# Kernel tuning notes

Measured on AMD Instinct MI355X. Metric: run time of the kernel, lower is better.

The kernel has to match this reference:

```python
import jax, jax.numpy as jnp
import numpy as np

D_MODEL = 512
N_HEADS = 8
D_HEAD = D_MODEL // N_HEADS
EPS = 1e-5


def layer_norm(x, g, b):
    mu = jnp.mean(x, axis=-1, keepdims=True)
    var = jnp.mean(jnp.square(x - mu), axis=-1, keepdims=True)
    return (x - mu) * jax.lax.rsqrt(var + EPS) * g + b


def setup_inputs() -> dict:
    key = jax.random.key(0)
    ks = jax.random.split(key, 8)
    B, L, D = 2, 4096, D_MODEL
    x = jax.random.normal(ks[0], (B, L, D), dtype=jnp.float32)
    # monotonically increasing event timestamps (hours)
    timestamps = jnp.sort(jax.random.uniform(ks[1], (B, L), dtype=jnp.float32) * 1000.0, axis=-1)
    mask = jnp.ones((B, L), dtype=jnp.float32)
    s = 0.02
    return {
        "x": x,
        "timestamps": timestamps,
        "mask": mask,
        "ln1_g": jnp.ones((D,), jnp.float32),
        "ln1_b": jnp.zeros((D,), jnp.float32),
        "w_qkv": jax.random.normal(ks[2], (3 * D, D), jnp.float32) * s,
        "w_out": jax.random.normal(ks[3], (D, D), jnp.float32) * s,
        "decay_rate": jnp.ones((N_HEADS,), jnp.float32) * 0.01,
        "ln2_g": jnp.ones((D,), jnp.float32),
        "ln2_b": jnp.zeros((D,), jnp.float32),
        "w_ff1": jax.random.normal(ks[4], (4 * D, D), jnp.float32) * s,
        "w_ff2": jax.random.normal(ks[5], (D, 4 * D), jnp.float32) * s,
    }


def reference(x, timestamps, mask, ln1_g, ln1_b, w_qkv, w_out, decay_rate, ln2_g, ln2_b, w_ff1, w_ff2):
    B, L, D = x.shape
    H, dh = N_HEADS, D_HEAD
    scale = dh ** (-0.5)

    xn = layer_norm(x, ln1_g, ln1_b)
    qkv = (xn @ w_qkv.T).reshape(B, L, 3, H, dh).transpose(2, 0, 3, 1, 4)  # [3,B,H,L,dh]
    q, k, v = qkv[0], qkv[1], qkv[2]

    attn = jnp.einsum("bhid,bhjd->bhij", q, k) * scale  # [B,H,L,L]

    # temporal-decay bias
    t_diff = jnp.abs(timestamps[:, None, :, None] - timestamps[:, None, None, :]) / 24.0  # [B,1,L,L]
    decay = jax.nn.softplus(decay_rate)[None, :, None, None]  # [1,H,1,1]
    attn = attn - decay * t_diff

    # causal mask
    causal = jnp.triu(jnp.ones((L, L), dtype=bool), k=1)
    attn = jnp.where(causal[None, None], -jnp.inf, attn)

    # padding mask over keys
    pad = (mask == 0)[:, None, None, :]  # [B,1,1,L]
    attn = jnp.where(pad, -jnp.inf, attn)

    attn = jax.nn.softmax(attn, axis=-1)
    out = jnp.einsum("bhij,bhjd->bhid", attn, v).transpose(0, 2, 1, 3).reshape(B, L, D)

    x = x + out @ w_out.T
    h = layer_norm(x, ln2_g, ln2_b)
    x = x + jax.nn.silu(h @ w_ff1.T) @ w_ff2.T
    return x
```

## Files before the change

kernel.cpp:

```cpp
#include <hip/hip_runtime.h>
#include <hip/hip_bf16.h>
#include <cmath>


#define L_SEQ 4096
#define D_MODEL 512
#define N_HEADS 8
#define D_HEAD 64
#define QKV_LD 1536

typedef __attribute__((ext_vector_type(8))) short bf16x8;
typedef __attribute__((ext_vector_type(4))) float f32x4;
typedef __attribute__((ext_vector_type(4))) unsigned u32x4;

__device__ __forceinline__ __hip_bfloat16 f2bf(float v) { return __float2bfloat16(v); }

__device__ __forceinline__ void gl_lds16(const __hip_bfloat16* g, __hip_bfloat16* l) {
  __builtin_amdgcn_global_load_lds((__attribute__((address_space(1))) void*)g,
                                   (__attribute__((address_space(3))) void*)l, 16, 0, 0);
}

__global__ __launch_bounds__(256) void cvt4b_kernel(const float* __restrict__ s0, __hip_bfloat16* __restrict__ d0,
                                                    const float* __restrict__ s1, __hip_bfloat16* __restrict__ d1,
                                                    const float* __restrict__ s2, __hip_bfloat16* __restrict__ d2,
                                                    const float* __restrict__ s3, __hip_bfloat16* __restrict__ d3,
                                                    const float* __restrict__ ts,
                                                    const float* __restrict__ mask,
                                                    const float* __restrict__ decay_rate,
                                                    float* __restrict__ biasH) {
  const int i = blockIdx.x * 256 + threadIdx.x;
  if (i < 786432) {
    const float* s;
    __hip_bfloat16* d;
    int off;
    if (i < 196608) { s = s0; d = d0; off = i; }
    else if (i < 262144) { s = s1; d = d1; off = i - 196608; }
    else if (i < 524288) { s = s2; d = d2; off = i - 262144; }
    else { s = s3; d = d3; off = i - 524288; }
    const float4 v = ((const float4*)s)[off];
    d[4 * off + 0] = f2bf(v.x);
    d[4 * off + 1] = f2bf(v.y);
    d[4 * off + 2] = f2bf(v.z);
    d[4 * off + 3] = f2bf(v.w);
  } else {
    const int idx = i - 786432;
    const int col = idx & 4095;
    const int h = (idx >> 12) & 7;
    const int b = idx >> 15;
    const float LOG2E = 1.4426950408889634f;
    const float dfac = log1pf(expf(decay_rate[h])) * (1.0f / 24.0f) * LOG2E;
    const float m = mask[b * 4096 + col];
    biasH[idx] = dfac * ts[b * 4096 + col] + (m != 0.f ? 0.f : -1e30f);
  }
}

__global__ __launch_bounds__(256) void ln_kernel(const float* __restrict__ x,
                                                 const float* __restrict__ g,
                                                 const float* __restrict__ b,
                                                 __hip_bfloat16* __restrict__ out) {
  const int row = blockIdx.x;
  const int t = threadIdx.x;
  const float* xr = x + (size_t)row * D_MODEL;
  float v0 = xr[t];
  float v1 = xr[t + 256];
  float s = v0 + v1;
  float qq = v0 * v0 + v1 * v1;
  for (int off = 32; off > 0; off >>= 1) {
    s += __shfl_xor(s, off);
    qq += __shfl_xor(qq, off);
  }
  __shared__ float red[8];
  const int wid = t >> 6;
  if ((t & 63) == 0) { red[wid] = s; red[4 + wid] = qq; }
  __syncthreads();
  s = red[0] + red[1] + red[2] + red[3];
  qq = red[4] + red[5] + red[6] + red[7];
  const float mu = s * (1.0f / 512.0f);
  const float var = fmaxf(qq * (1.0f / 512.0f) - mu * mu, 0.0f);
  const float rstd = rsqrtf(var + 1e-5f);
  __hip_bfloat16* orow = out + (size_t)row * D_MODEL;
  orow[t] = f2bf((v0 - mu) * rstd * g[t] + b[t]);
  orow[t + 256] = f2bf((v1 - mu) * rstd * g[t + 256] + b[t + 256]);
}

__global__ __launch_bounds__(256) void vtrans_kernel(const __hip_bfloat16* __restrict__ qkv,
                                                     __hip_bfloat16* __restrict__ vt) {
  const int gid = blockIdx.x * 256 + threadIdx.x;
  const int l = gid & 4095;
  const int bg = gid >> 12;
  const int b = bg >> 6, g = bg & 63;
  const int h = g >> 3, dg = (g & 7) * 8;
  const __hip_bfloat16* src = qkv + (size_t)(b * L_SEQ + l) * QKV_LD + 1024 + h * 64 + dg;
  bf16x8 v = *(const bf16x8*)src;
  const int kin = l & 63;
  const int sl = (kin & 0x23) | ((kin & 0x10) >> 2) | ((kin & 0x0c) << 1);
  const size_t dbase = (size_t)((b * 8 + h) * 64 + dg) * L_SEQ + (l & ~63) + sl;
  for (int j = 0; j < 8; j++)
    vt[dbase + (size_t)j * L_SEQ] = ((const __hip_bfloat16*)&v)[j];
}

template <int EPI>
__global__ __launch_bounds__(256) void gemm_kernel(const __hip_bfloat16* __restrict__ A,
                                                   const __hip_bfloat16* __restrict__ B,
                                                   int M, int N, int K,
                                                   const float* __restrict__ aux,
                                                   void* __restrict__ C) {
  __shared__ __align__(16) __hip_bfloat16 As[2][128 * 32];
  __shared__ __align__(16) __hip_bfloat16 Bs[2][128 * 32];
  const int tid = threadIdx.x;
  const int lane = tid & 63, w = tid >> 6;
  const int m0 = blockIdx.y * 128, n0 = blockIdx.x * 128;
  const int wm = (w >> 1) * 64, wn = (w & 1) * 64;
  const int r = lane & 15, q = lane >> 4;

  f32x4 acc[4][4];
  const f32x4 zz = {0.f, 0.f, 0.f, 0.f};
  for (int i = 0; i < 4; i++)
    for (int j = 0; j < 4; j++) acc[i][j] = zz;

  const int c0 = tid, c1 = 256 + tid;
  const int row0 = c0 >> 2, kb0 = (c0 & 3) * 8;
  const int row1 = c1 >> 2, kb1 = (c1 & 3) * 8;

#define GEMM_STAGE(k0, buf)                                                     \
  do {                                                                          \
    gl_lds16(A + (size_t)(m0 + row0) * K + ((k0) + kb0), &As[buf][c0 * 8]);     \
    gl_lds16(B + (size_t)(n0 + row0) * K + ((k0) + kb0), &Bs[buf][c0 * 8]);     \
    gl_lds16(A + (size_t)(m0 + row1) * K + ((k0) + kb1), &As[buf][c1 * 8]);     \
    gl_lds16(B + (size_t)(n0 + row1) * K + ((k0) + kb1), &Bs[buf][c1 * 8]);     \
  } while (0)

  GEMM_STAGE(0, 0);
  const int niter = K >> 5;
  for (int it = 0; it < niter; it++) {
    const int cur = it & 1;
    if (it + 1 < niter) {
      GEMM_STAGE((it + 1) << 5, cur ^ 1);
      asm volatile("s_waitcnt vmcnt(4)" ::: "memory");
    } else {
      asm volatile("s_waitcnt vmcnt(0)" ::: "memory");
    }
    __builtin_amdgcn_s_barrier();
    bf16x8 af[4], bfr[4];
    for (int mi = 0; mi < 4; mi++)
      af[mi] = *(const bf16x8*)(&As[cur][(wm + mi * 16 + r) * 32 + q * 8]);
    for (int ni = 0; ni < 4; ni++)
      bfr[ni] = *(const bf16x8*)(&Bs[cur][(wn + ni * 16 + r) * 32 + q * 8]);
    for (int mi = 0; mi < 4; mi++)
      for (int ni = 0; ni < 4; ni++)
        acc[mi][ni] = __builtin_amdgcn_mfma_f32_16x16x32_bf16(af[mi], bfr[ni], acc[mi][ni], 0, 0, 0);
    __builtin_amdgcn_s_barrier();
  }
#undef GEMM_STAGE

  for (int mi = 0; mi < 4; mi++)
    for (int ni = 0; ni < 4; ni++)
      for (int j = 0; j < 4; j++) {
        const int gm = m0 + wm + mi * 16 + q * 4 + j;
        const int gn = n0 + wn + ni * 16 + r;
        float v = acc[mi][ni][j];
        const size_t idx = (size_t)gm * N + gn;
        if (EPI == 0) {
          ((__hip_bfloat16*)C)[idx] = f2bf(v);
        } else {
          v = v / (1.0f + expf(-v));
          ((__hip_bfloat16*)C)[idx] = f2bf(v);
        }
      }
}

__global__ __launch_bounds__(256) void gemm_res64_kernel(const __hip_bfloat16* __restrict__ A,
                                                         const __hip_bfloat16* __restrict__ B,
                                                         int M, int N, int K,
                                                         const float* __restrict__ aux,
                                                         float* __restrict__ C) {
  __shared__ __align__(16) __hip_bfloat16 As[2][64 * 32];
  __shared__ __align__(16) __hip_bfloat16 Bs[2][128 * 32];
  const int tid = threadIdx.x;
  const int lane = tid & 63, w = tid >> 6;
  const int m0 = blockIdx.y * 64, n0 = blockIdx.x * 128;
  const int wm = (w >> 1) * 32, wn = (w & 1) * 64;
  const int r = lane & 15, q = lane >> 4;

  f32x4 acc[2][4];
  const f32x4 zz = {0.f, 0.f, 0.f, 0.f};
  for (int i = 0; i < 2; i++)
    for (int j = 0; j < 4; j++) acc[i][j] = zz;

  const int rowA = tid >> 2, kbA = (tid & 3) * 8;
  const int c0 = tid, c1 = 256 + tid;
  const int rowB0 = c0 >> 2, kb0 = (c0 & 3) * 8;
  const int rowB1 = c1 >> 2, kb1 = (c1 & 3) * 8;

#define GEMM_STAGE64(k0, buf)                                                    \
  do {                                                                           \
    gl_lds16(A + (size_t)(m0 + rowA) * K + ((k0) + kbA), &As[buf][tid * 8]);     \
    gl_lds16(B + (size_t)(n0 + rowB0) * K + ((k0) + kb0), &Bs[buf][c0 * 8]);     \
    gl_lds16(B + (size_t)(n0 + rowB1) * K + ((k0) + kb1), &Bs[buf][c1 * 8]);     \
  } while (0)

  GEMM_STAGE64(0, 0);
  const int niter = K >> 5;
  for (int it = 0; it < niter; it++) {
    const int cur = it & 1;
    if (it + 1 < niter) {
      GEMM_STAGE64((it + 1) << 5, cur ^ 1);
      asm volatile("s_waitcnt vmcnt(3)" ::: "memory");
    } else {
      asm volatile("s_waitcnt vmcnt(0)" ::: "memory");
    }
    __builtin_amdgcn_s_barrier();
    bf16x8 af[2], bfr[4];
    for (int mi = 0; mi < 2; mi++)
      af[mi] = *(const bf16x8*)(&As[cur][(wm + mi * 16 + r) * 32 + q * 8]);
    for (int ni = 0; ni < 4; ni++)
      bfr[ni] = *(const bf16x8*)(&Bs[cur][(wn + ni * 16 + r) * 32 + q * 8]);
    for (int mi = 0; mi < 2; mi++)
      for (int ni = 0; ni < 4; ni++)
        acc[mi][ni] = __builtin_amdgcn_mfma_f32_16x16x32_bf16(af[mi], bfr[ni], acc[mi][ni], 0, 0, 0);
    __builtin_amdgcn_s_barrier();
  }
#undef GEMM_STAGE64

  for (int mi = 0; mi < 2; mi++)
    for (int ni = 0; ni < 4; ni++)
      for (int j = 0; j < 4; j++) {
        const int gm = m0 + wm + mi * 16 + q * 4 + j;
        const int gn = n0 + wn + ni * 16 + r;
        const size_t idx = (size_t)gm * N + gn;
        C[idx] = acc[mi][ni][j] + aux[idx];
      }
}

__device__ __forceinline__ void stage_kv8(int w, int lane, int key0,
                                          const __hip_bfloat16* __restrict__ Kg,
                                          const __hip_bfloat16* __restrict__ Vg,
                                          __hip_bfloat16* Ks, __hip_bfloat16* Vs) {
  const int row_in = lane >> 3;
  const int cs = (lane & 7) ^ row_in;
  const int row = w * 8 + row_in;
  gl_lds16(Kg + (size_t)(key0 + row) * QKV_LD + cs * 8, Ks + w * 512 + lane * 8);
  gl_lds16(Vg + (size_t)row * L_SEQ + key0 + cs * 8, Vs + w * 512 + lane * 8);
}

template <bool CAUSAL>
__device__ __forceinline__ void attn_tile(int key0, int lw0, int r, int q,
                                          const __hip_bfloat16* Ks,
                                          const __hip_bfloat16* Vs,
                                          const float* biasLds,
                                          float scale2,
                                          const bf16x8& qf0, const bf16x8& qf1,
                                          const bf16x8& onesf,
                                          f32x4* o, f32x4& ls) {
  const int r7 = r & 7;
  const f32x4 zz = {0.f, 0.f, 0.f, 0.f};
  f32x4 bias4[4];
#pragma unroll
  for (int hc = 0; hc < 4; hc++)
    bias4[hc] = *(const f32x4*)(biasLds + key0 + hc * 16 + q * 4);
  f32x4 s[4];
  __builtin_amdgcn_s_setprio(1);
#pragma unroll
  for (int hc = 0; hc < 4; hc++) {
    const __hip_bfloat16* kr = Ks + (hc * 16 + r) * 64;
    bf16x8 k0 = *(const bf16x8*)(kr + ((q ^ r7) * 8));
    bf16x8 k1 = *(const bf16x8*)(kr + (((q + 4) ^ r7) * 8));
    f32x4 a = zz;
    a = __builtin_amdgcn_mfma_f32_16x16x32_bf16(k0, qf0, a, 0, 0, 0);
    a = __builtin_amdgcn_mfma_f32_16x16x32_bf16(k1, qf1, a, 0, 0, 0);
    s[hc] = a;
  }
  __builtin_amdgcn_s_setprio(0);
  float p[4][4];
#pragma unroll
  for (int hc = 0; hc < 4; hc++)
#pragma unroll
    for (int j = 0; j < 4; j++) {
      const float v = fmaf(s[hc][j], scale2, bias4[hc][j]);
      float pv = exp2f(v);
      if (CAUSAL) pv = (key0 + hc * 16 + q * 4 + j <= lw0 + r) ? pv : 0.f;
      p[hc][j] = pv;
    }
  bf16x8 pa[2];
#pragma unroll
  for (int kc = 0; kc < 2; kc++) {
    u32x4 pw;
    unsigned w0, w1, w2, w3;
    asm("v_cvt_pk_bf16_f32 %0, %1, %2" : "=v"(w0) : "v"(p[2 * kc][0]), "v"(p[2 * kc][1]));
    asm("v_cvt_pk_bf16_f32 %0, %1, %2" : "=v"(w1) : "v"(p[2 * kc][2]), "v"(p[2 * kc][3]));
    asm("v_cvt_pk_bf16_f32 %0, %1, %2" : "=v"(w2) : "v"(p[2 * kc + 1][0]), "v"(p[2 * kc + 1][1]));
    asm("v_cvt_pk_bf16_f32 %0, %1, %2" : "=v"(w3) : "v"(p[2 * kc + 1][2]), "v"(p[2 * kc + 1][3]));
    pw[0] = w0; pw[1] = w1; pw[2] = w2; pw[3] = w3;
    pa[kc] = *(bf16x8*)&pw;
  }
  __builtin_amdgcn_s_setprio(1);
#pragma unroll
  for (int kc = 0; kc < 2; kc++) {
#pragma unroll
    for (int c = 0; c < 4; c++) {
      const __hip_bfloat16* vr = Vs + (c * 16 + r) * 64 + (((kc * 4 + q) ^ r7) * 8);
      bf16x8 vf = *(const bf16x8*)vr;
      o[c] = __builtin_amdgcn_mfma_f32_16x16x32_bf16(pa[kc], vf, o[c], 0, 0, 0);
    }
    ls = __builtin_amdgcn_mfma_f32_16x16x32_bf16(pa[kc], onesf, ls, 0, 0, 0);
  }
  __builtin_amdgcn_s_setprio(0);
}

__global__ __launch_bounds__(512, 2) void attn_kernel(const __hip_bfloat16* __restrict__ qkv,
                                                      const __hip_bfloat16* __restrict__ vt,
                                                      const float* __restrict__ biasH,
                                                      __hip_bfloat16* __restrict__ out) {
  const int blk = blockIdx.x;
  const int bh = blk & 15;
  const int pr = blk >> 4;
  const int b = bh >> 3, h = bh & 7;
  const int tid = threadIdx.x, lane = tid & 63, w = tid >> 6;
  const int grp = w >> 2, wg = w & 3;
  const int qi = grp ? (63 - pr) : pr;
  const int l0 = qi * 64;
  const int lw0 = l0 + wg * 16;
  const int r = lane & 15, q = lane >> 4;

  __shared__ __align__(16) __hip_bfloat16 Ksm[2][64 * 64];
  __shared__ __align__(16) __hip_bfloat16 Vsm[2][64 * 64];
  __shared__ __align__(16) float biasLds[4096];

  const float LOG2E = 1.4426950408889634f;
  const float scale2 = 0.125f * LOG2E;

  const __hip_bfloat16* Kg = qkv + (size_t)b * L_SEQ * QKV_LD + 512 + h * 64;
  const __hip_bfloat16* Vg = vt + (size_t)bh * 64 * L_SEQ;
  const float* biasHp = biasH + (size_t)bh * L_SEQ;

  stage_kv8(w, lane, 0, Kg, Vg, Ksm[0], Vsm[0]);
#pragma unroll
  for (int ii = 0; ii < 2; ii++) {
    const int fo = (w * 2 + ii) * 256;
    gl_lds16((const __hip_bfloat16*)(biasHp + fo + lane * 4),
             (__hip_bfloat16*)(biasLds + fo + lane * 4));
  }

  bf16x8 qf0, qf1;
  {
    const __hip_bfloat16* qrow = qkv + (size_t)(b * L_SEQ + lw0 + r) * QKV_LD + h * 64 + q * 8;
    qf0 = *(const bf16x8*)qrow;
    qf1 = *(const bf16x8*)(qrow + 32);
  }

  const f32x4 zz = {0.f, 0.f, 0.f, 0.f};
  f32x4 o[4];
  for (int c = 0; c < 4; c++) o[c] = zz;
  f32x4 ls = zz;

  bf16x8 onesf;
  for (int i = 0; i < 8; i++) ((short*)&onesf)[i] = (short)0x3F80;

  const int ntA = pr + 1;
  const int ntB = 64 - pr;
  const int nt = grp ? ntB : ntA;

  for (int t = 0; t < ntB; t++) {
    const int cur = t & 1;
    if (t + 1 < ntB) {
      stage_kv8(w, lane, (t + 1) << 6, Kg, Vg, Ksm[cur ^ 1], Vsm[cur ^ 1]);
      asm volatile("s_waitcnt vmcnt(2)" ::: "memory");
    } else {
      asm volatile("s_waitcnt vmcnt(0)" ::: "memory");
    }
    __builtin_amdgcn_s_barrier();
    if (t < nt) {
      if (t == nt - 1)
        attn_tile<true>(t << 6, lw0, r, q, Ksm[cur], Vsm[cur], biasLds, scale2, qf0, qf1,
                        onesf, o, ls);
      else
        attn_tile<false>(t << 6, lw0, r, q, Ksm[cur], Vsm[cur], biasLds, scale2, qf0, qf1,
                         onesf, o, ls);
    }
    __builtin_amdgcn_s_barrier();
  }

  float invj[4];
  for (int j = 0; j < 4; j++) invj[j] = 1.0f / ls[j];
  for (int c = 0; c < 4; c++)
    for (int j = 0; j < 4; j++) {
      const int rowg = lw0 + q * 4 + j;
      out[(size_t)(b * L_SEQ + rowg) * D_MODEL + h * 64 + c * 16 + r] = f2bf(o[c][j] * invj[j]);
    }
}

extern "C" void kernel_launch(void* const* d_in, const int* in_sizes, int n_in,
                              void* d_out, int out_size, void* d_ws, size_t ws_size,
                              hipStream_t stream) {
  const float* x = (const float*)d_in[0];
  const float* ts = (const float*)d_in[1];
  const float* mask = (const float*)d_in[2];
  const float* ln1_g = (const float*)d_in[3];
  const float* ln1_b = (const float*)d_in[4];
  const float* w_qkv = (const float*)d_in[5];
  const float* w_out = (const float*)d_in[6];
  const float* decay = (const float*)d_in[7];
  const float* ln2_g = (const float*)d_in[8];
  const float* ln2_b = (const float*)d_in[9];
  const float* w_ff1 = (const float*)d_in[10];
  const float* w_ff2 = (const float*)d_in[11];

  char* ws = (char*)d_ws;
  __hip_bfloat16* wqkv_b = (__hip_bfloat16*)(ws + 0);
  __hip_bfloat16* wout_b = (__hip_bfloat16*)(ws + 1572864);
  __hip_bfloat16* wff1_b = (__hip_bfloat16*)(ws + 2097152);
  __hip_bfloat16* wff2_b = (__hip_bfloat16*)(ws + 4194304);
  __hip_bfloat16* xn = (__hip_bfloat16*)(ws + 6291456);
  __hip_bfloat16* vt = (__hip_bfloat16*)(ws + 6291456);
  __hip_bfloat16* qkv = (__hip_bfloat16*)(ws + 14680064);
  __hip_bfloat16* attnout = (__hip_bfloat16*)(ws + 39845888);
  __hip_bfloat16* h = attnout;
  __hip_bfloat16* ff1out = (__hip_bfloat16*)(ws + 6291456);
  float* x2 = (float*)(ws + 48234496);
  float* biasH = (float*)(ws + 48234496);
  float* out = (float*)d_out;

  const int M = 2 * L_SEQ;

  cvt4b_kernel<<<dim3(3328), dim3(256), 0, stream>>>(w_qkv, wqkv_b, w_out, wout_b,
                                                     w_ff1, wff1_b, w_ff2, wff2_b,
                                                     ts, mask, decay, biasH);

  ln_kernel<<<dim3(M), dim3(256), 0, stream>>>(x, ln1_g, ln1_b, xn);
  gemm_kernel<0><<<dim3(12, 64), dim3(256), 0, stream>>>(xn, wqkv_b, M, 1536, 512, nullptr, qkv);
  vtrans_kernel<<<dim3(2048), dim3(256), 0, stream>>>(qkv, vt);
  attn_kernel<<<dim3(512), dim3(512), 0, stream>>>(qkv, vt, biasH, attnout);
  gemm_res64_kernel<<<dim3(4, 128), dim3(256), 0, stream>>>(attnout, wout_b, M, 512, 512, x, x2);
  ln_kernel<<<dim3(M), dim3(256), 0, stream>>>(x2, ln2_g, ln2_b, h);
  gemm_kernel<2><<<dim3(16, 64), dim3(256), 0, stream>>>(h, wff1_b, M, 2048, 512, nullptr, ff1out);
  gemm_res64_kernel<<<dim3(4, 128), dim3(256), 0, stream>>>(ff1out, wff2_b, M, 512, 2048, x2, out);
}
```

Before: 293.9 us.

## Triple-buffer GEMM K-loop and pair adjacent query tiles per attention block

Both GEMM kernels move from double to triple buffering in LDS, prefetching two K-steps ahead with adjusted vmcnt waits, so global-load latency is hidden further. The attention kernel is remapped so each block processes two query-tile phases: an early pair of adjacent tiles, then a late pair. The K/V prefetch for the second phase is chained from the end of the first. This balances causal work between the two wave groups and halves the grid to 256 blocks. The cost is more LDS per GEMM block and only one attention block per CU, which leaves fewer resident waves to hide latency.

```diff
diff --git a/kernel.cpp b/kernel.cpp
--- a/kernel.cpp
+++ b/kernel.cpp
@@ -105,8 +105,8 @@
                                                    int M, int N, int K,
                                                    const float* __restrict__ aux,
                                                    void* __restrict__ C) {
-  __shared__ __align__(16) __hip_bfloat16 As[2][128 * 32];
-  __shared__ __align__(16) __hip_bfloat16 Bs[2][128 * 32];
+  __shared__ __align__(16) __hip_bfloat16 As[3][128 * 32];
+  __shared__ __align__(16) __hip_bfloat16 Bs[3][128 * 32];
   const int tid = threadIdx.x;
   const int lane = tid & 63, w = tid >> 6;
   const int m0 = blockIdx.y * 128, n0 = blockIdx.x * 128;
@@ -131,11 +131,15 @@
   } while (0)
 
   GEMM_STAGE(0, 0);
+  GEMM_STAGE(32, 1);
   const int niter = K >> 5;
   for (int it = 0; it < niter; it++) {
-    const int cur = it & 1;
-    if (it + 1 < niter) {
-      GEMM_STAGE((it + 1) << 5, cur ^ 1);
+    const int cur = it % 3;
+    const int rem = niter - 1 - it;
+    if (rem >= 2) {
+      GEMM_STAGE((it + 2) << 5, (it + 2) % 3);
+      asm volatile("s_waitcnt vmcnt(8)" ::: "memory");
+    } else if (rem == 1) {
       asm volatile("s_waitcnt vmcnt(4)" ::: "memory");
     } else {
       asm volatile("s_waitcnt vmcnt(0)" ::: "memory");
@@ -174,8 +178,8 @@
                                                          int M, int N, int K,
                                                          const float* __restrict__ aux,
                                                          float* __restrict__ C) {
-  __shared__ __align__(16) __hip_bfloat16 As[2][64 * 32];
-  __shared__ __align__(16) __hip_bfloat16 Bs[2][128 * 32];
+  __shared__ __align__(16) __hip_bfloat16 As[3][64 * 32];
+  __shared__ __align__(16) __hip_bfloat16 Bs[3][128 * 32];
   const int tid = threadIdx.x;
   const int lane = tid & 63, w = tid >> 6;
   const int m0 = blockIdx.y * 64, n0 = blockIdx.x * 128;
@@ -200,11 +204,15 @@
   } while (0)
 
   GEMM_STAGE64(0, 0);
+  GEMM_STAGE64(32, 1);
   const int niter = K >> 5;
   for (int it = 0; it < niter; it++) {
-    const int cur = it & 1;
-    if (it + 1 < niter) {
-      GEMM_STAGE64((it + 1) << 5, cur ^ 1);
+    const int cur = it % 3;
+    const int rem = niter - 1 - it;
+    if (rem >= 2) {
+      GEMM_STAGE64((it + 2) << 5, (it + 2) % 3);
+      asm volatile("s_waitcnt vmcnt(6)" ::: "memory");
+    } else if (rem == 1) {
       asm volatile("s_waitcnt vmcnt(3)" ::: "memory");
     } else {
       asm volatile("s_waitcnt vmcnt(0)" ::: "memory");
@@ -313,14 +321,18 @@
                                                       __hip_bfloat16* __restrict__ out) {
   const int blk = blockIdx.x;
   const int bh = blk & 15;
-  const int pr = blk >> 4;
+  const int i2 = blk >> 4;
   const int b = bh >> 3, h = bh & 7;
   const int tid = threadIdx.x, lane = tid & 63, w = tid >> 6;
   const int grp = w >> 2, wg = w & 3;
-  const int qi = grp ? (63 - pr) : pr;
-  const int l0 = qi * 64;
-  const int lw0 = l0 + wg * 16;
   const int r = lane & 15, q = lane >> 4;
+
+  const int qi1 = 2 * i2 + grp;
+  const int qi2 = 62 - 2 * i2 + grp;
+  const int s1 = 2 * i2 + 2;
+  const int s2 = 64 - 2 * i2;
+  const int nt1 = qi1 + 1, nt2 = qi2 + 1;
+  const int lw01 = qi1 * 64 + wg * 16, lw02 = qi2 * 64 + wg * 16;
 
   __shared__ __align__(16) __hip_bfloat16 Ksm[2][64 * 64];
   __shared__ __align__(16) __hip_bfloat16 Vsm[2][64 * 64];
@@ -341,11 +353,14 @@
              (__hip_bfloat16*)(biasLds + fo + lane * 4));
   }
 
-  bf16x8 qf0, qf1;
+  bf16x8 qf10, qf11, qf20, qf21;
   {
-    const __hip_bfloat16* qrow = qkv + (size_t)(b * L_SEQ + lw0 + r) * QKV_LD + h * 64 + q * 8;
-    qf0 = *(const bf16x8*)qrow;
-    qf1 = *(const bf16x8*)(qrow + 32);
+    const __hip_bfloat16* qr1 = qkv + (size_t)(b * L_SEQ + lw01 + r) * QKV_LD + h * 64 + q * 8;
+    qf10 = *(const bf16x8*)qr1;
+    qf11 = *(const bf16x8*)(qr1 + 32);
+    const __hip_bfloat16* qr2 = qkv + (size_t)(b * L_SEQ + lw02 + r) * QKV_LD + h * 64 + q * 8;
+    qf20 = *(const bf16x8*)qr2;
+    qf21 = *(const bf16x8*)(qr2 + 32);
   }
 
   const f32x4 zz = {0.f, 0.f, 0.f, 0.f};
@@ -356,37 +371,64 @@
   bf16x8 onesf;
   for (int i = 0; i < 8; i++) ((short*)&onesf)[i] = (short)0x3F80;
 
-  const int ntA = pr + 1;
-  const int ntB = 64 - pr;
-  const int nt = grp ? ntB : ntA;
-
-  for (int t = 0; t < ntB; t++) {
+  for (int t = 0; t < s1; t++) {
     const int cur = t & 1;
-    if (t + 1 < ntB) {
+    const int nk = (t + 1 < s1) ? (t + 1) : 0;
+    stage_kv8(w, lane, nk << 6, Kg, Vg, Ksm[cur ^ 1], Vsm[cur ^ 1]);
+    asm volatile("s_waitcnt vmcnt(2)" ::: "memory");
+    __builtin_amdgcn_s_barrier();
+    if (t < nt1) {
+      if (t == nt1 - 1)
+        attn_tile<true>(t << 6, lw01, r, q, Ksm[cur], Vsm[cur], biasLds, scale2, qf10, qf11,
+                        onesf, o, ls);
+      else
+        attn_tile<false>(t << 6, lw01, r, q, Ksm[cur], Vsm[cur], biasLds, scale2, qf10, qf11,
+                         onesf, o, ls);
+    }
+    __builtin_amdgcn_s_barrier();
+  }
+
+  {
+    float invj[4];
+    for (int j = 0; j < 4; j++) invj[j] = 1.0f / ls[j];
+    for (int c = 0; c < 4; c++)
+      for (int j = 0; j < 4; j++) {
+        const int rowg = lw01 + q * 4 + j;
+        out[(size_t)(b * L_SEQ + rowg) * D_MODEL + h * 64 + c * 16 + r] = f2bf(o[c][j] * invj[j]);
+      }
+    for (int c = 0; c < 4; c++) o[c] = zz;
+    ls = zz;
+  }
+
+  for (int t = 0; t < s2; t++) {
+    const int cur = (s1 + t) & 1;
+    if (t + 1 < s2) {
       stage_kv8(w, lane, (t + 1) << 6, Kg, Vg, Ksm[cur ^ 1], Vsm[cur ^ 1]);
       asm volatile("s_waitcnt vmcnt(2)" ::: "memory");
     } else {
       asm volatile("s_waitcnt vmcnt(0)" ::: "memory");
     }
     __builtin_amdgcn_s_barrier();
-    if (t < nt) {
-      if (t == nt - 1)
-        attn_tile<true>(t << 6, lw0, r, q, Ksm[cur], Vsm[cur], biasLds, scale2, qf0, qf1,
+    if (t < nt2) {
+      if (t == nt2 - 1)
+        attn_tile<true>(t << 6, lw02, r, q, Ksm[cur], Vsm[cur], biasLds, scale2, qf20, qf21,
                         onesf, o, ls);
       else
-        attn_tile<false>(t << 6, lw0, r, q, Ksm[cur], Vsm[cur], biasLds, scale2, qf0, qf1,
+        attn_tile<false>(t << 6, lw02, r, q, Ksm[cur], Vsm[cur], biasLds, scale2, qf20, qf21,
                          onesf, o, ls);
     }
     __builtin_amdgcn_s_barrier();
   }
 
-  float invj[4];
-  for (int j = 0; j < 4; j++) invj[j] = 1.0f / ls[j];
-  for (int c = 0; c < 4; c++)
-    for (int j = 0; j < 4; j++) {
-      const int rowg = lw0 + q * 4 + j;
-      out[(size_t)(b * L_SEQ + rowg) * D_MODEL + h * 64 + c * 16 + r] = f2bf(o[c][j] * invj[j]);
-    }
+  {
+    float invj[4];
+    for (int j = 0; j < 4; j++) invj[j] = 1.0f / ls[j];
+    for (int c = 0; c < 4; c++)
+      for (int j = 0; j < 4; j++) {
+        const int rowg = lw02 + q * 4 + j;
+        out[(size_t)(b * L_SEQ + rowg) * D_MODEL + h * 64 + c * 16 + r] = f2bf(o[c][j] * invj[j]);
+      }
+  }
 }
 
 extern "C" void kernel_launch(void* const* d_in, const int* in_sizes, int n_in,
@@ -429,7 +471,7 @@
   ln_kernel<<<dim3(M), dim3(256), 0, stream>>>(x, ln1_g, ln1_b, xn);
   gemm_kernel<0><<<dim3(12, 64), dim3(256), 0, stream>>>(xn, wqkv_b, M, 1536, 512, nullptr, qkv);
   vtrans_kernel<<<dim3(2048), dim3(256), 0, stream>>>(qkv, vt);
-  attn_kernel<<<dim3(512), dim3(512), 0, stream>>>(qkv, vt, biasH, attnout);
+  attn_kernel<<<dim3(256), dim3(512), 0, stream>>>(qkv, vt, biasH, attnout);
   gemm_res64_kernel<<<dim3(4, 128), dim3(256), 0, stream>>>(attnout, wout_b, M, 512, 512, x, x2);
   ln_kernel<<<dim3(M), dim3(256), 0, stream>>>(x2, ln2_g, ln2_b, h);
   gemm_kernel<2><<<dim3(16, 64), dim3(256), 0, stream>>>(h, wff1_b, M, 2048, 512, nullptr, ff1out);
```

New measurement: 308.7 us. 5.0% more time.

## Double attention key tile to 128 and use raw v_exp_f32

Applied to the files above, without the earlier changes.

Widens each K/V staging tile from 64 to 128 keys, so the loop runs half as many iterations and issues half as many barrier pairs. The V tile layout and swizzle change to match. Softmax exponentials now use the raw v_exp_f32 instruction instead of exp2f, skipping its range handling. Launch bounds now ask for 4 blocks per CU, but LDS use grows to about 80KB per block, which likely caps real occupancy. The larger tile also puts more work on the diagonal tile, where masked lanes are computed and then zeroed.

```diff
diff --git a/kernel.cpp b/kernel.cpp
--- a/kernel.cpp
+++ b/kernel.cpp
@@ -14,6 +14,12 @@
 typedef __attribute__((ext_vector_type(4))) unsigned u32x4;
 
 __device__ __forceinline__ __hip_bfloat16 f2bf(float v) { return __float2bfloat16(v); }
+
+__device__ __forceinline__ float exp2_raw(float x) {
+  float r;
+  asm("v_exp_f32 %0, %1" : "=v"(r) : "v"(x));
+  return r;
+}
 
 __device__ __forceinline__ void gl_lds16(const __hip_bfloat16* g, __hip_bfloat16* l) {
   __builtin_amdgcn_global_load_lds((__attribute__((address_space(1))) void*)g,
@@ -232,36 +238,44 @@
       }
 }
 
-__device__ __forceinline__ void stage_kv8(int w, int lane, int key0,
-                                          const __hip_bfloat16* __restrict__ Kg,
-                                          const __hip_bfloat16* __restrict__ Vg,
-                                          __hip_bfloat16* Ks, __hip_bfloat16* Vs) {
-  const int row_in = lane >> 3;
-  const int cs = (lane & 7) ^ row_in;
-  const int row = w * 8 + row_in;
-  gl_lds16(Kg + (size_t)(key0 + row) * QKV_LD + cs * 8, Ks + w * 512 + lane * 8);
-  gl_lds16(Vg + (size_t)row * L_SEQ + key0 + cs * 8, Vs + w * 512 + lane * 8);
+__device__ __forceinline__ void stage_kv128(int w, int lane, int key0,
+                                            const __hip_bfloat16* __restrict__ Kg,
+                                            const __hip_bfloat16* __restrict__ Vg,
+                                            __hip_bfloat16* Ks, __hip_bfloat16* Vs) {
+  const int krow_in = lane >> 3;
+  const int kcs = (lane & 7) ^ krow_in;
+  const int vrow_in = lane >> 4;
+  const int vch = lane & 15;
+#pragma unroll
+  for (int ii = 0; ii < 2; ii++) {
+    const int i = w * 2 + ii;
+    const int krow = i * 8 + krow_in;
+    gl_lds16(Kg + (size_t)(key0 + krow) * QKV_LD + kcs * 8, Ks + i * 512 + lane * 8);
+    const int vrow = i * 4 + vrow_in;
+    const int vcs = vch ^ (vrow & 7);
+    gl_lds16(Vg + (size_t)vrow * L_SEQ + key0 + vcs * 8, Vs + i * 512 + lane * 8);
+  }
 }
 
 template <bool CAUSAL>
-__device__ __forceinline__ void attn_tile(int key0, int lw0, int r, int q,
-                                          const __hip_bfloat16* Ks,
-                                          const __hip_bfloat16* Vs,
-                                          const float* biasLds,
-                                          float scale2,
-                                          const bf16x8& qf0, const bf16x8& qf1,
-                                          const bf16x8& onesf,
-                                          f32x4* o, f32x4& ls) {
+__device__ __forceinline__ void attn_tile128(int key0, int lw0, int r, int q,
+                                             const __hip_bfloat16* Ks,
+                                             const __hip_bfloat16* Vs,
+                                             const float* biasLds,
+                                             float scale2,
+                                             const bf16x8& qf0, const bf16x8& qf1,
+                                             const bf16x8& onesf,
+                                             f32x4* o, f32x4& ls) {
   const int r7 = r & 7;
   const f32x4 zz = {0.f, 0.f, 0.f, 0.f};
-  f32x4 bias4[4];
-#pragma unroll
-  for (int hc = 0; hc < 4; hc++)
+  f32x4 bias4[8];
+#pragma unroll
+  for (int hc = 0; hc < 8; hc++)
     bias4[hc] = *(const f32x4*)(biasLds + key0 + hc * 16 + q * 4);
-  f32x4 s[4];
+  f32x4 s[8];
   __builtin_amdgcn_s_setprio(1);
 #pragma unroll
-  for (int hc = 0; hc < 4; hc++) {
+  for (int hc = 0; hc < 8; hc++) {
     const __hip_bfloat16* kr = Ks + (hc * 16 + r) * 64;
     bf16x8 k0 = *(const bf16x8*)(kr + ((q ^ r7) * 8));
     bf16x8 k1 = *(const bf16x8*)(kr + (((q + 4) ^ r7) * 8));
@@ -271,19 +285,18 @@
     s[hc] = a;
   }
   __builtin_amdgcn_s_setprio(0);
-  float p[4][4];
-#pragma unroll
-  for (int hc = 0; hc < 4; hc++)
+  float p[8][4];
+#pragma unroll
+  for (int hc = 0; hc < 8; hc++)
 #pragma unroll
     for (int j = 0; j < 4; j++) {
-      const float v = fmaf(s[hc][j], scale2, bias4[hc][j]);
-      float pv = exp2f(v);
+      float pv = exp2_raw(fmaf(s[hc][j], scale2, bias4[hc][j]));
       if (CAUSAL) pv = (key0 + hc * 16 + q * 4 + j <= lw0 + r) ? pv : 0.f;
       p[hc][j] = pv;
     }
-  bf16x8 pa[2];
-#pragma unroll
-  for (int kc = 0; kc < 2; kc++) {
+  bf16x8 pa[4];
+#pragma unroll
+  for (int kc = 0; kc < 4; kc++) {
     u32x4 pw;
     unsigned w0, w1, w2, w3;
     asm("v_cvt_pk_bf16_f32 %0, %1, %2" : "=v"(w0) : "v"(p[2 * kc][0]), "v"(p[2 * kc][1]));
@@ -295,10 +308,10 @@
   }
   __builtin_amdgcn_s_setprio(1);
 #pragma unroll
-  for (int kc = 0; kc < 2; kc++) {
+  for (int kc = 0; kc < 4; kc++) {
 #pragma unroll
     for (int c = 0; c < 4; c++) {
-      const __hip_bfloat16* vr = Vs + (c * 16 + r) * 64 + (((kc * 4 + q) ^ r7) * 8);
+      const __hip_bfloat16* vr = Vs + (c * 16 + r) * 128 + (((kc * 4 + q) ^ r7) * 8);
       bf16x8 vf = *(const bf16x8*)vr;
       o[c] = __builtin_amdgcn_mfma_f32_16x16x32_bf16(pa[kc], vf, o[c], 0, 0, 0);
     }
@@ -307,7 +320,7 @@
   __builtin_amdgcn_s_setprio(0);
 }
 
-__global__ __launch_bounds__(512, 2) void attn_kernel(const __hip_bfloat16* __restrict__ qkv,
+__global__ __launch_bounds__(512, 4) void attn_kernel(const __hip_bfloat16* __restrict__ qkv,
                                                       const __hip_bfloat16* __restrict__ vt,
                                                       const float* __restrict__ biasH,
                                                       __hip_bfloat16* __restrict__ out) {
@@ -322,8 +335,8 @@
   const int lw0 = l0 + wg * 16;
   const int r = lane & 15, q = lane >> 4;
 
-  __shared__ __align__(16) __hip_bfloat16 Ksm[2][64 * 64];
-  __shared__ __align__(16) __hip_bfloat16 Vsm[2][64 * 64];
+  __shared__ __align__(16) __hip_bfloat16 Ksm[2][128 * 64];
+  __shared__ __align__(16) __hip_bfloat16 Vsm[2][64 * 128];
   __shared__ __align__(16) float biasLds[4096];
 
   const float LOG2E = 1.4426950408889634f;
@@ -333,7 +346,7 @@
   const __hip_bfloat16* Vg = vt + (size_t)bh * 64 * L_SEQ;
   const float* biasHp = biasH + (size_t)bh * L_SEQ;
 
-  stage_kv8(w, lane, 0, Kg, Vg, Ksm[0], Vsm[0]);
+  stage_kv128(w, lane, 0, Kg, Vg, Ksm[0], Vsm[0]);
 #pragma unroll
   for (int ii = 0; ii < 2; ii++) {
     const int fo = (w * 2 + ii) * 256;
@@ -356,26 +369,26 @@
   bf16x8 onesf;
   for (int i = 0; i < 8; i++) ((short*)&onesf)[i] = (short)0x3F80;
 
-  const int ntA = pr + 1;
-  const int ntB = 64 - pr;
+  const int ntA = (pr >> 1) + 1;
+  const int ntB = ((63 - pr) >> 1) + 1;
   const int nt = grp ? ntB : ntA;
 
   for (int t = 0; t < ntB; t++) {
     const int cur = t & 1;
     if (t + 1 < ntB) {
-      stage_kv8(w, lane, (t + 1) << 6, Kg, Vg, Ksm[cur ^ 1], Vsm[cur ^ 1]);
-      asm volatile("s_waitcnt vmcnt(2)" ::: "memory");
+      stage_kv128(w, lane, (t + 1) << 7, Kg, Vg, Ksm[cur ^ 1], Vsm[cur ^ 1]);
+      asm volatile("s_waitcnt vmcnt(4)" ::: "memory");
     } else {
       asm volatile("s_waitcnt vmcnt(0)" ::: "memory");
     }
     __builtin_amdgcn_s_barrier();
     if (t < nt) {
       if (t == nt - 1)
-        attn_tile<true>(t << 6, lw0, r, q, Ksm[cur], Vsm[cur], biasLds, scale2, qf0, qf1,
-                        onesf, o, ls);
+        attn_tile128<true>(t << 7, lw0, r, q, Ksm[cur], Vsm[cur], biasLds, scale2, qf0, qf1,
+                           onesf, o, ls);
       else
-        attn_tile<false>(t << 6, lw0, r, q, Ksm[cur], Vsm[cur], biasLds, scale2, qf0, qf1,
-                         onesf, o, ls);
+        attn_tile128<false>(t << 7, lw0, r, q, Ksm[cur], Vsm[cur], biasLds, scale2, qf0, qf1,
+                            onesf, o, ls);
     }
     __builtin_amdgcn_s_barrier();
   }
```

Result: faster. 268.0 us (-8.8%).
